# Kernel optimization log

Measured on AMD Instinct MI355X. Metric: run time of the kernel, lower is better.

## Reference

```python
import jax, jax.numpy as jnp
import numpy as np

N = 1 << 20          # number of sample points (rays x samples)
ENC = 32             # hash-grid encoded dim (16 levels x 2 features)
HID = 64
GEO = 15


def setup_inputs() -> dict:
    key = jax.random.key(0)
    ks = jax.random.split(key, 16)
    sc = lambda fan_in: 1.0 / np.sqrt(fan_in)
    return {
        "x": jax.random.normal(ks[0], (N, ENC), jnp.float32),
        "d": jax.random.normal(ks[1], (N, ENC), jnp.float32),
        # sigma net: ENC -> 64 -> 64 -> 1+GEO, bias-free, stored [in, out]
        "Ws0": jax.random.normal(ks[2], (ENC, HID), jnp.float32) * sc(ENC),
        "Ws1": jax.random.normal(ks[3], (HID, HID), jnp.float32) * sc(HID),
        "Ws2": jax.random.normal(ks[4], (HID, 1 + GEO), jnp.float32) * sc(HID),
        # color net: ENC+GEO -> 64 -> 64 -> 64 -> 3, bias-free
        "Wc0": jax.random.normal(ks[5], (ENC + GEO, HID), jnp.float32) * sc(ENC + GEO),
        "Wc1": jax.random.normal(ks[6], (HID, HID), jnp.float32) * sc(HID),
        "Wc2": jax.random.normal(ks[7], (HID, HID), jnp.float32) * sc(HID),
        "Wc3": jax.random.normal(ks[8], (HID, 3), jnp.float32) * sc(HID),
    }


def reference(x, d, Ws0, Ws1, Ws2, Wc0, Wc1, Wc2, Wc3):
    # sigma network: ReLU after EVERY layer (including the last, as in source)
    h = x
    for W in (Ws0, Ws1, Ws2):
        h = jax.nn.relu(h @ W)
    sigma = h[..., 0]            # [N]
    geo_feat = h[..., 1:]        # [N, GEO]

    # color network: ReLU on all but last layer, then sigmoid
    h = jnp.concatenate([d, geo_feat], axis=-1)   # [N, ENC+GEO]
    color_ws = (Wc0, Wc1, Wc2, Wc3)
    for i, W in enumerate(color_ws):
        h = h @ W
        if i != len(color_ws) - 1:
            h = jax.nn.relu(h)
    color = jax.nn.sigmoid(h)    # [N, 3]
    return color, sigma
```

## Files before the change

kernel.cpp:

```cpp
#include <hip/hip_runtime.h>
#include <hip/hip_bf16.h>

typedef short s8v  __attribute__((ext_vector_type(8)));
typedef float f4v  __attribute__((ext_vector_type(4)));
typedef float f16v __attribute__((ext_vector_type(16)));

#define MFMA32 __builtin_amdgcn_mfma_f32_32x32x16_bf16

constexpr int OFF_W0T  = 0;
constexpr int OFF_W1T  = 2560;
constexpr int OFF_W2T  = 7168;
constexpr int OFF_WC0T = 9472;
constexpr int OFF_WC1T = 14080;
constexpr int OFF_WC2T = 18688;
constexpr int OFF_WC3T = 23296;
constexpr int SMEM_EL  = 25600;

static __device__ __forceinline__ short bf2s(__hip_bfloat16 h) {
    union { __hip_bfloat16 b; short s; } u; u.b = h; return u.s;
}

__global__ __launch_bounds__(512, 4)
void rf_fused(const void* __restrict__ xv,
              const void* __restrict__ dv,
              const void* __restrict__ Ws0,
              const void* __restrict__ Ws1,
              const void* __restrict__ Ws2,
              const void* __restrict__ Wc0,
              const void* __restrict__ Wc1,
              const void* __restrict__ Wc2,
              const void* __restrict__ Wc3,
              void* __restrict__ outp,
              int npts)
{
    __shared__ __align__(16) short smem[SMEM_EL];
    __shared__ int cls_cnt;
    const int t = threadIdx.x;

    if (t == 0) cls_cnt = 0;
    __syncthreads();
    {
        unsigned short w = ((const unsigned short*)xv)[2 * t];
        int e = (w >> 7) & 0xFF;
        if (e >= 110 && e <= 140) atomicAdd(&cls_cnt, 1);
    }
    __syncthreads();
    const bool isbf = (cls_cnt >= 256);

    auto ldw = [&](const void* p, int idx) -> short {
        if (isbf) return ((const short*)p)[idx];
        return bf2s(__float2bfloat16(((const float*)p)[idx]));
    };

    for (int i = t; i < 2048; i += 512) { int k = i >> 6, n = i & 63; smem[OFF_W0T + n*40 + k] = ldw(Ws0, i); }
    for (int i = t; i < 4096; i += 512) { int k = i >> 6, n = i & 63; smem[OFF_W1T + n*72 + k] = ldw(Ws1, i); }
    for (int i = t; i < 2048; i += 512) {
        int n = i >> 6, k = i & 63;
        smem[OFF_W2T + n*72 + k] = (n < 16) ? ldw(Ws2, k*16 + n) : (short)0;
    }
    for (int i = t; i < 4096; i += 512) {
        int n = i >> 6, k = i & 63;
        short v = 0;
        if (k < 32)                 v = ldw(Wc0, k*64 + n);
        else if (k >= 33 && k < 48) v = ldw(Wc0, (k-1)*64 + n);
        smem[OFF_WC0T + n*72 + k] = v;
    }
    for (int i = t; i < 4096; i += 512) { int k = i >> 6, n = i & 63; smem[OFF_WC1T + n*72 + k] = ldw(Wc1, i); }
    for (int i = t; i < 4096; i += 512) { int k = i >> 6, n = i & 63; smem[OFF_WC2T + n*72 + k] = ldw(Wc2, i); }
    for (int i = t; i < 2048; i += 512) {
        int n = i >> 6, k = i & 63;
        smem[OFF_WC3T + n*72 + k] = (n < 3) ? ldw(Wc3, k*3 + n) : (short)0;
    }
    __syncthreads();

    const int lane = t & 63;
    const int wv   = t >> 6;
    const int l5   = lane & 31;
    const int hi   = lane >> 5;
    const f16v zf16 = {0.f,0.f,0.f,0.f,0.f,0.f,0.f,0.f,
                       0.f,0.f,0.f,0.f,0.f,0.f,0.f,0.f};

    s8v w2f[4];
    #pragma unroll
    for (int kc = 0; kc < 4; kc++)
        w2f[kc] = *(const s8v*)(smem + OFF_W2T + l5*72 + kc*16 + hi*8);

    auto loadRow8f = [&](const void* p, int eoff) -> s8v {
        const float* f = (const float*)p + eoff;
        f4v f0 = *(const f4v*)f;
        f4v f1 = *(const f4v*)(f + 4);
        s8v r;
        #pragma unroll
        for (int j = 0; j < 4; j++) {
            r[j]     = bf2s(__float2bfloat16(f0[j]));
            r[j + 4] = bf2s(__float2bfloat16(f1[j]));
        }
        return r;
    };
    auto putOut = [&](int idx, float v) {
        if (isbf) ((short*)outp)[idx] = bf2s(__float2bfloat16(v));
        else      ((float*)outp)[idx] = v;
    };
    auto cvtpk = [](float lo, float hiV) -> unsigned int {
        unsigned int r;
        asm("v_cvt_pk_bf16_f32 %0, %1, %2" : "=v"(r) : "v"(lo), "v"(hiV));
        return r;
    };
    auto swap32 = [](unsigned int &x, unsigned int &y) {
        asm("v_permlane32_swap_b32 %0, %1" : "+v"(x), "+v"(y));
    };

    auto redist32 = [&](const f16v &a0, const f16v &a1, s8v (&fr)[4]) {
        unsigned int Q[2][4][2];
        #pragma unroll
        for (int tt = 0; tt < 2; tt++) {
            const f16v &a = tt ? a1 : a0;
            #pragma unroll
            for (int aa = 0; aa < 4; aa++)
                #pragma unroll
                for (int e = 0; e < 2; e++)
                    Q[tt][aa][e] = cvtpk(fmaxf(a[4*aa + 2*e], 0.f),
                                         fmaxf(a[4*aa + 2*e + 1], 0.f));
        }
        #pragma unroll
        for (int tt = 0; tt < 2; tt++)
            #pragma unroll
            for (int A = 0; A < 2; A++)
                #pragma unroll
                for (int e = 0; e < 2; e++)
                    swap32(Q[tt][2*A][e], Q[tt][2*A + 1][e]);
        #pragma unroll
        for (int c = 0; c < 4; c++) {
            const int tt = c >> 1, A = c & 1;
            union { unsigned int u[4]; s8v v; } fu;
            fu.u[0] = Q[tt][2*A][0];     fu.u[1] = Q[tt][2*A][1];
            fu.u[2] = Q[tt][2*A + 1][0]; fu.u[3] = Q[tt][2*A + 1][1];
            fr[c] = fu.v;
        }
    };
    auto redistJ = [&](const f16v &a, s8v &fg) {
        unsigned int Q[2][2];
        #pragma unroll
        for (int aa = 0; aa < 2; aa++)
            #pragma unroll
            for (int e = 0; e < 2; e++)
                Q[aa][e] = cvtpk(fmaxf(a[4*aa + 2*e], 0.f),
                                 fmaxf(a[4*aa + 2*e + 1], 0.f));
        #pragma unroll
        for (int e = 0; e < 2; e++) swap32(Q[0][e], Q[1][e]);
        union { unsigned int u[4]; s8v v; } fu;
        fu.u[0] = Q[0][0]; fu.u[1] = Q[0][1];
        fu.u[2] = Q[1][0]; fu.u[3] = Q[1][1];
        fg = fu.v;
    };

    auto layer64 = [&](int woff, const s8v (&b)[4], f16v (&o)[2]) {
        #pragma unroll
        for (int mt = 0; mt < 2; mt++) {
            f16v c = zf16;
            #pragma unroll
            for (int kc = 0; kc < 4; kc++) {
                s8v a = *(const s8v*)(smem + woff + (mt*32 + l5)*72 + kc*16 + hi*8);
                c = MFMA32(a, b[kc], c, 0, 0, 0);
            }
            o[mt] = c;
        }
    };

    const int ntiles = npts / 32;
    const int nw     = gridDim.x * 8;
    int tile = blockIdx.x * 8 + wv;

    auto loadB2 = [&](const void* p, int r0, s8v (&f)[2]) {
        #pragma unroll
        for (int kc = 0; kc < 2; kc++) {
            const int off = (r0 + l5)*32 + kc*16 + hi*8;
            f[kc] = isbf ? *(const s8v*)((const short*)p + off) : loadRow8f(p, off);
        }
    };

    s8v xb[2];
    if (tile < ntiles) loadB2(xv, tile*32, xb);

    #pragma unroll 1
    for (; tile < ntiles; tile += nw) {
        const int r0  = tile * 32;
        const int nxt = tile + nw;

        s8v db[2];
        loadB2(dv, r0, db);

        f16v h[2];
        #pragma unroll
        for (int mt = 0; mt < 2; mt++) {
            f16v c = zf16;
            #pragma unroll
            for (int kc = 0; kc < 2; kc++) {
                s8v a = *(const s8v*)(smem + OFF_W0T + (mt*32 + l5)*40 + kc*16 + hi*8);
                c = MFMA32(a, xb[kc], c, 0, 0, 0);
            }
            h[mt] = c;
        }

        s8v xbn[2];
        if (nxt < ntiles) loadB2(xv, nxt*32, xbn);

        s8v bfr[4];
        redist32(h[0], h[1], bfr);

        layer64(OFF_W1T, bfr, h);
        redist32(h[0], h[1], bfr);

        f16v s3 = zf16;
        #pragma unroll
        for (int kc = 0; kc < 4; kc++)
            s3 = MFMA32(w2f[kc], bfr[kc], s3, 0, 0, 0);

        if (hi == 0) putOut(3*npts + r0 + l5, fmaxf(s3[0], 0.f));

        s8v geo;
        redistJ(s3, geo);

        #pragma unroll
        for (int mt = 0; mt < 2; mt++) {
            const int base = OFF_WC0T + (mt*32 + l5)*72;
            f16v c = zf16;
            c = MFMA32(*(const s8v*)(smem + base +  0 + hi*8), db[0], c, 0, 0, 0);
            c = MFMA32(*(const s8v*)(smem + base + 16 + hi*8), db[1], c, 0, 0, 0);
            c = MFMA32(*(const s8v*)(smem + base + 32 + hi*8), geo,   c, 0, 0, 0);
            h[mt] = c;
        }
        redist32(h[0], h[1], bfr);

        layer64(OFF_WC1T, bfr, h);
        redist32(h[0], h[1], bfr);

        layer64(OFF_WC2T, bfr, h);
        redist32(h[0], h[1], bfr);

        f16v c7 = zf16;
        #pragma unroll
        for (int kc = 0; kc < 4; kc++) {
            s8v a = *(const s8v*)(smem + OFF_WC3T + l5*72 + kc*16 + hi*8);
            c7 = MFMA32(a, bfr[kc], c7, 0, 0, 0);
        }
        if (hi == 0) {
            const int base = (r0 + l5) * 3;
            #pragma unroll
            for (int r = 0; r < 3; r++) {
                float sg = 1.0f / (1.0f + __expf(-c7[r]));
                putOut(base + r, sg);
            }
        }

        xb[0] = xbn[0]; xb[1] = xbn[1];
    }
}

extern "C" void kernel_launch(void* const* d_in, const int* in_sizes, int n_in,
                              void* d_out, int out_size, void* d_ws, size_t ws_size,
                              hipStream_t stream) {
    const int npts = in_sizes[0] / 32;
    rf_fused<<<512, 512, 0, stream>>>(d_in[0], d_in[1], d_in[2], d_in[3], d_in[4],
                                      d_in[5], d_in[6], d_in[7], d_in[8],
                                      d_out, npts);
}
```

Before: 312.0 us.

## Prefetch d tile, stagger wave start, and raise priority around MFMA chains

Prefetches the next tile's d input one iteration ahead, as is already done for x. It clamps the prefetch index so the loads run unconditionally. LDS weight fragments are hoisted ahead of each MFMA chain, and s_setprio is raised around the chains so matrix work from different waves interleaves better with memory work. Waves also sleep for a staggered time at startup so they fall out of phase, at the cost of some startup delay and higher register pressure from the extra prefetch buffers.

```diff
diff --git a/kernel.cpp b/kernel.cpp
--- a/kernel.cpp
+++ b/kernel.cpp
@@ -80,6 +80,11 @@
     const f16v zf16 = {0.f,0.f,0.f,0.f,0.f,0.f,0.f,0.f,
                        0.f,0.f,0.f,0.f,0.f,0.f,0.f,0.f};
 
+    {
+        const int slot = wv + 8 * (blockIdx.x & 1);
+        for (int i = 0; i < slot; ++i) __builtin_amdgcn_s_sleep(8);
+    }
+
     s8v w2f[4];
     #pragma unroll
     for (int kc = 0; kc < 4; kc++)
@@ -157,12 +162,17 @@
     auto layer64 = [&](int woff, const s8v (&b)[4], f16v (&o)[2]) {
         #pragma unroll
         for (int mt = 0; mt < 2; mt++) {
+            s8v a0 = *(const s8v*)(smem + woff + (mt*32 + l5)*72 +  0 + hi*8);
+            s8v a1 = *(const s8v*)(smem + woff + (mt*32 + l5)*72 + 16 + hi*8);
+            s8v a2 = *(const s8v*)(smem + woff + (mt*32 + l5)*72 + 32 + hi*8);
+            s8v a3 = *(const s8v*)(smem + woff + (mt*32 + l5)*72 + 48 + hi*8);
+            __builtin_amdgcn_s_setprio(1);
             f16v c = zf16;
-            #pragma unroll
-            for (int kc = 0; kc < 4; kc++) {
-                s8v a = *(const s8v*)(smem + woff + (mt*32 + l5)*72 + kc*16 + hi*8);
-                c = MFMA32(a, b[kc], c, 0, 0, 0);
-            }
+            c = MFMA32(a0, b[0], c, 0, 0, 0);
+            c = MFMA32(a1, b[1], c, 0, 0, 0);
+            c = MFMA32(a2, b[2], c, 0, 0, 0);
+            c = MFMA32(a3, b[3], c, 0, 0, 0);
+            __builtin_amdgcn_s_setprio(0);
             o[mt] = c;
         }
     };
@@ -179,31 +189,30 @@
         }
     };
 
-    s8v xb[2];
-    if (tile < ntiles) loadB2(xv, tile*32, xb);
+    s8v xb[2], db[2];
+    if (tile < ntiles) { loadB2(xv, tile*32, xb); loadB2(dv, tile*32, db); }
 
     #pragma unroll 1
     for (; tile < ntiles; tile += nw) {
-        const int r0  = tile * 32;
-        const int nxt = tile + nw;
-
-        s8v db[2];
-        loadB2(dv, r0, db);
+        const int r0   = tile * 32;
+        const int nxt  = tile + nw;
+        const int nclp = (nxt < ntiles) ? nxt : tile;
 
         f16v h[2];
         #pragma unroll
         for (int mt = 0; mt < 2; mt++) {
+            s8v a0 = *(const s8v*)(smem + OFF_W0T + (mt*32 + l5)*40 +  0 + hi*8);
+            s8v a1 = *(const s8v*)(smem + OFF_W0T + (mt*32 + l5)*40 + 16 + hi*8);
+            __builtin_amdgcn_s_setprio(1);
             f16v c = zf16;
-            #pragma unroll
-            for (int kc = 0; kc < 2; kc++) {
-                s8v a = *(const s8v*)(smem + OFF_W0T + (mt*32 + l5)*40 + kc*16 + hi*8);
-                c = MFMA32(a, xb[kc], c, 0, 0, 0);
-            }
+            c = MFMA32(a0, xb[0], c, 0, 0, 0);
+            c = MFMA32(a1, xb[1], c, 0, 0, 0);
+            __builtin_amdgcn_s_setprio(0);
             h[mt] = c;
         }
 
         s8v xbn[2];
-        if (nxt < ntiles) loadB2(xv, nxt*32, xbn);
+        loadB2(xv, nclp*32, xbn);
 
         s8v bfr[4];
         redist32(h[0], h[1], bfr);
@@ -211,10 +220,12 @@
         layer64(OFF_W1T, bfr, h);
         redist32(h[0], h[1], bfr);
 
+        __builtin_amdgcn_s_setprio(1);
         f16v s3 = zf16;
         #pragma unroll
         for (int kc = 0; kc < 4; kc++)
             s3 = MFMA32(w2f[kc], bfr[kc], s3, 0, 0, 0);
+        __builtin_amdgcn_s_setprio(0);
 
         if (hi == 0) putOut(3*npts + r0 + l5, fmaxf(s3[0], 0.f));
 
@@ -224,12 +235,21 @@
         #pragma unroll
         for (int mt = 0; mt < 2; mt++) {
             const int base = OFF_WC0T + (mt*32 + l5)*72;
+            s8v a0 = *(const s8v*)(smem + base +  0 + hi*8);
+            s8v a1 = *(const s8v*)(smem + base + 16 + hi*8);
+            s8v a2 = *(const s8v*)(smem + base + 32 + hi*8);
+            __builtin_amdgcn_s_setprio(1);
             f16v c = zf16;
-            c = MFMA32(*(const s8v*)(smem + base +  0 + hi*8), db[0], c, 0, 0, 0);
-            c = MFMA32(*(const s8v*)(smem + base + 16 + hi*8), db[1], c, 0, 0, 0);
-            c = MFMA32(*(const s8v*)(smem + base + 32 + hi*8), geo,   c, 0, 0, 0);
+            c = MFMA32(a0, db[0], c, 0, 0, 0);
+            c = MFMA32(a1, db[1], c, 0, 0, 0);
+            c = MFMA32(a2, geo,   c, 0, 0, 0);
+            __builtin_amdgcn_s_setprio(0);
             h[mt] = c;
         }
+
+        s8v dbn[2];
+        loadB2(dv, nclp*32, dbn);
+
         redist32(h[0], h[1], bfr);
 
         layer64(OFF_WC1T, bfr, h);
@@ -238,12 +258,14 @@
         layer64(OFF_WC2T, bfr, h);
         redist32(h[0], h[1], bfr);
 
+        __builtin_amdgcn_s_setprio(1);
         f16v c7 = zf16;
         #pragma unroll
         for (int kc = 0; kc < 4; kc++) {
             s8v a = *(const s8v*)(smem + OFF_WC3T + l5*72 + kc*16 + hi*8);
             c7 = MFMA32(a, bfr[kc], c7, 0, 0, 0);
         }
+        __builtin_amdgcn_s_setprio(0);
         if (hi == 0) {
             const int base = (r0 + l5) * 3;
             #pragma unroll
@@ -254,6 +276,7 @@
         }
 
         xb[0] = xbn[0]; xb[1] = xbn[1];
+        db[0] = dbn[0]; db[1] = dbn[1];
     }
 }
 
```

Result: no change. 313.8 us (+0.6%).
